# Kernel optimization log

Measured on AMD Instinct MI355X. Metric: run time of the kernel, lower is better.

Reference implementation:

```python
import jax, jax.numpy as jnp
import numpy as np

N_NODES = 10000
N_EDGES = 160000
NUM_REL = 16
NUM_BLOCKS = 32
BLOCK_SIZE = 4  # input_dim 128 = 32 * 4
INPUT_DIM = NUM_BLOCKS * BLOCK_SIZE


def setup_inputs() -> dict:
    key = jax.random.key(0)
    ks = jax.random.split(key, 6)
    std = float(np.sqrt(2.0) / (2 * BLOCK_SIZE))  # matches reset_parameters
    return {
        "x": jax.random.normal(ks[0], (N_NODES, INPUT_DIM), dtype=jnp.float32),
        "node_keep_mask": jnp.ones((N_NODES,), dtype=bool),
        "source": jax.random.randint(ks[1], (N_EDGES,), 0, N_NODES),
        "target": jax.random.randint(ks[2], (N_EDGES,), 0, N_NODES),
        "edge_type": jax.random.randint(ks[3], (N_EDGES,), 0, NUM_REL),
        "edge_weights": jax.random.uniform(ks[4], (N_EDGES,), dtype=jnp.float32),
        "blocks": jax.random.normal(ks[5], (NUM_REL + 1, NUM_BLOCKS, BLOCK_SIZE, BLOCK_SIZE), dtype=jnp.float32) * std,
    }


def reference(x, node_keep_mask, source, target, edge_type, edge_weights, blocks):
    n = x.shape[0]
    _, nb, bs, _ = blocks.shape
    xb = x.reshape(n, nb, bs)  # (N, B, bs)
    # self-loop transform with last block set; dropped-out nodes stay zero
    self_msg = jnp.einsum('nbi,bij->nbj', xb, blocks[-1])
    out = jnp.where(node_keep_mask[:, None, None], self_msg, 0.0)
    # symmetrize edges: messages flow both directions with same relation/weight
    src2 = jnp.concatenate([source, target])
    tgt2 = jnp.concatenate([target, source])
    et2 = jnp.concatenate([edge_type, edge_type])
    ew2 = jnp.concatenate([edge_weights, edge_weights])
    # per-edge block-diagonal matmul: gather relation blocks then 4x4 block GEMMs
    w_e = blocks[et2]                              # (2E, B, bs, bs)
    m = jnp.einsum('ebi,ebij->ebj', xb[src2], w_e)  # (2E, B, bs)
    m = m * ew2[:, None, None]
    out = out + jax.ops.segment_sum(m, tgt2, num_segments=n)
    return out.reshape(n, nb * bs)
```

## Files before the change

### kernel.cpp

```cpp
#include <hip/hip_runtime.h>

#define INPUT_DIM 128
#define NB 32
#define BS 4
#define CAP 128
#define WSTRIDE 20
#define GBLOCKS 1280


__global__ void scatter_kernel(const int* __restrict__ src, const int* __restrict__ tgt,
                               const int* __restrict__ etype, const float* __restrict__ ew,
                               int* __restrict__ counts, int2* __restrict__ msg,
                               int n_edges) {
    int i = blockIdx.x * blockDim.x + threadIdx.x;
    if (i >= 2 * n_edges) return;
    int e = (i < n_edges) ? i : i - n_edges;
    int s, t;
    if (i < n_edges) { s = src[e]; t = tgt[e]; }
    else             { s = tgt[e]; t = src[e]; }
    int pk = s | (etype[e] << 16);
    float w = ew[e];
    int pos = atomicAdd(&counts[t], 1);
    msg[t * CAP + pos] = make_int2(pk, __float_as_int(w));
}

__global__ __launch_bounds__(256, 4)
void gather_kernel(const float* __restrict__ x,
                   const int* __restrict__ keep,
                   const float* __restrict__ blocks,
                   const int* __restrict__ counts,
                   const int2* __restrict__ msg,
                   float* __restrict__ out, int n_nodes) {
    __shared__ float Wlds[16 * NB * WSTRIDE];

    for (int i = threadIdx.x; i < 16 * NB * 4; i += 256) {
        int blk = i >> 2;
        int row = i & 3;
        *(float4*)&Wlds[blk * WSTRIDE + row * 4] = ((const float4*)blocks)[i];
    }
    __syncthreads();

    int lane = threadIdx.x & 63;
    int b = lane & 31;
    int slot = lane >> 5;
    int wave_id = (blockIdx.x * blockDim.x + threadIdx.x) >> 6;
    int n_waves = gridDim.x * (blockDim.x >> 6);

    #define DO_MSG(PK, W)                                                     \
        {                                                                     \
            int s_ = (PK) & 0xFFFF;                                           \
            int r_ = (PK) >> 16;                                              \
            const float* Wp_ = &Wlds[(r_ * NB + b) * WSTRIDE];                \
            const float4 c0 = *(const float4*)(Wp_ + 0);                      \
            const float4 c1 = *(const float4*)(Wp_ + 4);                      \
            const float4 c2 = *(const float4*)(Wp_ + 8);                      \
            const float4 c3 = *(const float4*)(Wp_ + 12);                     \
            const float4 xv = *(const float4*)(x + (size_t)s_ * INPUT_DIM + b * BS); \
            acc.x += (W) * (xv.x * c0.x + xv.y * c1.x + xv.z * c2.x + xv.w * c3.x); \
            acc.y += (W) * (xv.x * c0.y + xv.y * c1.y + xv.z * c2.y + xv.w * c3.y); \
            acc.z += (W) * (xv.x * c0.z + xv.y * c1.z + xv.z * c2.z + xv.w * c3.z); \
            acc.w += (W) * (xv.x * c0.w + xv.y * c1.w + xv.z * c2.w + xv.w * c3.w); \
        }

    for (int n = wave_id; n < n_nodes; n += n_waves) {
        float4 acc = make_float4(0.f, 0.f, 0.f, 0.f);

        if (slot == 0 && keep[n] != 0) {
            const float4 xv = *(const float4*)(x + (size_t)n * INPUT_DIM + b * BS);
            const float* Wp = blocks + (((size_t)16 * NB + b) << 4);
            const float4 c0 = *(const float4*)(Wp + 0);
            const float4 c1 = *(const float4*)(Wp + 4);
            const float4 c2 = *(const float4*)(Wp + 8);
            const float4 c3 = *(const float4*)(Wp + 12);
            acc.x = xv.x * c0.x + xv.y * c1.x + xv.z * c2.x + xv.w * c3.x;
            acc.y = xv.x * c0.y + xv.y * c1.y + xv.z * c2.y + xv.w * c3.y;
            acc.z = xv.x * c0.z + xv.y * c1.z + xv.z * c2.z + xv.w * c3.z;
            acc.w = xv.x * c0.w + xv.y * c1.w + xv.z * c2.w + xv.w * c3.w;
        }

        int cnt = counts[n];
        int base = n * CAP;
        int p = 0;
        for (; p + 4 <= cnt; p += 4) {
            int2 m0 = msg[base + p + slot];
            int2 m1 = msg[base + p + 2 + slot];
            float w0 = __int_as_float(m0.y);
            float w1 = __int_as_float(m1.y);
            DO_MSG(m0.x, w0);
            DO_MSG(m1.x, w1);
        }
        for (; p < cnt; p += 2) {
            if (p + slot < cnt) {
                int2 m = msg[base + p + slot];
                DO_MSG(m.x, __int_as_float(m.y));
            }
        }

        acc.x += __shfl_xor(acc.x, 32, 64);
        acc.y += __shfl_xor(acc.y, 32, 64);
        acc.z += __shfl_xor(acc.z, 32, 64);
        acc.w += __shfl_xor(acc.w, 32, 64);

        if (slot == 0)
            *(float4*)(out + (size_t)n * INPUT_DIM + b * BS) = acc;
    }
    #undef DO_MSG
}

extern "C" void kernel_launch(void* const* d_in, const int* in_sizes, int n_in,
                              void* d_out, int out_size, void* d_ws, size_t ws_size,
                              hipStream_t stream) {
    const float* x       = (const float*)d_in[0];
    const int* km        = (const int*)d_in[1];
    const int* source    = (const int*)d_in[2];
    const int* target    = (const int*)d_in[3];
    const int* edge_type = (const int*)d_in[4];
    const float* edge_w  = (const float*)d_in[5];
    const float* blocks  = (const float*)d_in[6];
    float* out           = (float*)d_out;

    int n_nodes = in_sizes[0] / INPUT_DIM;
    int n_edges = in_sizes[2];
    int n_msg   = 2 * n_edges;

    int* counts = (int*)d_ws;
    int2* msg   = (int2*)((char*)d_ws + 65536);

    hipMemsetAsync(counts, 0, n_nodes * sizeof(int), stream);
    scatter_kernel<<<(n_msg + 255) / 256, 256, 0, stream>>>(
        source, target, edge_type, edge_w, counts, msg, n_edges);
    gather_kernel<<<GBLOCKS, 256, 0, stream>>>(
        x, km, blocks, counts, msg, out, n_nodes);
}
```

Baseline: 119.0 us.

## Convert x and relation blocks to fp16 and use packed dot2 in gather

A prep kernel converts x to packed fp16 and also performs the edge scatter, with each thread handling both directions of one edge. The gather kernel stores the relation blocks in LDS as transposed fp16 pairs and computes each 4x4 block product with fdot2 instructions, halving the bytes of the random x gathers. This lowers precision of the inputs and weights, which may exceed tolerance, and adds a conversion pass over x.

```diff
diff --git a/kernel.cpp b/kernel.cpp
--- a/kernel.cpp
+++ b/kernel.cpp
@@ -4,39 +4,77 @@
 #define NB 32
 #define BS 4
 #define CAP 128
-#define WSTRIDE 20
+#define WSTRIDE_U 12
 #define GBLOCKS 1280
 
+typedef _Float16 h2 __attribute__((ext_vector_type(2)));
+union HU { unsigned int u; h2 h; };
 
-__global__ void scatter_kernel(const int* __restrict__ src, const int* __restrict__ tgt,
-                               const int* __restrict__ etype, const float* __restrict__ ew,
-                               int* __restrict__ counts, int2* __restrict__ msg,
-                               int n_edges) {
+__device__ inline unsigned int pack_f16(float a, float b) {
+    HU v; v.h = h2{(_Float16)a, (_Float16)b}; return v.u;
+}
+__device__ inline h2 as_h2(unsigned int u) { HU v; v.u = u; return v.h; }
+
+#if defined(__has_builtin) && __has_builtin(__builtin_amdgcn_fdot2)
+__device__ inline float dot2(h2 a, h2 b, float c) {
+    return __builtin_amdgcn_fdot2(a, b, c, false);
+}
+#else
+__device__ inline float dot2(h2 a, h2 b, float c) {
+    return (float)a.x * (float)b.x + (float)a.y * (float)b.y + c;
+}
+#endif
+
+
+__global__ void prep_kernel(const float* __restrict__ x, unsigned int* __restrict__ xh,
+                            const int* __restrict__ src, const int* __restrict__ tgt,
+                            const int* __restrict__ etype, const float* __restrict__ ew,
+                            int* __restrict__ counts, int2* __restrict__ msg,
+                            int n_edges, int nx8) {
     int i = blockIdx.x * blockDim.x + threadIdx.x;
-    if (i >= 2 * n_edges) return;
-    int e = (i < n_edges) ? i : i - n_edges;
-    int s, t;
-    if (i < n_edges) { s = src[e]; t = tgt[e]; }
-    else             { s = tgt[e]; t = src[e]; }
-    int pk = s | (etype[e] << 16);
-    float w = ew[e];
-    int pos = atomicAdd(&counts[t], 1);
-    msg[t * CAP + pos] = make_int2(pk, __float_as_int(w));
+    if (i < nx8) {
+        const float4 a = *(const float4*)(x + (size_t)i * 8);
+        const float4 b = *(const float4*)(x + (size_t)i * 8 + 4);
+        uint4 o;
+        o.x = pack_f16(a.x, a.y);
+        o.y = pack_f16(a.z, a.w);
+        o.z = pack_f16(b.x, b.y);
+        o.w = pack_f16(b.z, b.w);
+        *(uint4*)(xh + (size_t)i * 4) = o;
+    }
+    if (i < n_edges) {
+        int s = src[i], t = tgt[i];
+        int pk_base = etype[i] << 16;
+        int wbits = __float_as_int(ew[i]);
+        int pf = atomicAdd(&counts[t], 1);
+        msg[t * CAP + pf] = make_int2(s | pk_base, wbits);
+        int pb = atomicAdd(&counts[s], 1);
+        msg[s * CAP + pb] = make_int2(t | pk_base, wbits);
+    }
 }
 
 __global__ __launch_bounds__(256, 4)
 void gather_kernel(const float* __restrict__ x,
+                   const unsigned int* __restrict__ xh,
                    const int* __restrict__ keep,
                    const float* __restrict__ blocks,
                    const int* __restrict__ counts,
                    const int2* __restrict__ msg,
                    float* __restrict__ out, int n_nodes) {
-    __shared__ float Wlds[16 * NB * WSTRIDE];
+    __shared__ unsigned int Wlds[16 * NB * WSTRIDE_U];
 
-    for (int i = threadIdx.x; i < 16 * NB * 4; i += 256) {
-        int blk = i >> 2;
-        int row = i & 3;
-        *(float4*)&Wlds[blk * WSTRIDE + row * 4] = ((const float4*)blocks)[i];
+    for (int bi = threadIdx.x; bi < 16 * NB; bi += 256) {
+        const float4 r0 = ((const float4*)blocks)[bi * 4 + 0];
+        const float4 r1 = ((const float4*)blocks)[bi * 4 + 1];
+        const float4 r2 = ((const float4*)blocks)[bi * 4 + 2];
+        const float4 r3 = ((const float4*)blocks)[bi * 4 + 3];
+        uint4 q0, q1;
+        q0.x = pack_f16(r0.x, r1.x); q0.y = pack_f16(r2.x, r3.x);
+        q0.z = pack_f16(r0.y, r1.y); q0.w = pack_f16(r2.y, r3.y);
+        q1.x = pack_f16(r0.z, r1.z); q1.y = pack_f16(r2.z, r3.z);
+        q1.z = pack_f16(r0.w, r1.w); q1.w = pack_f16(r2.w, r3.w);
+        *(uint4*)&Wlds[bi * WSTRIDE_U + 0] = q0;
+        *(uint4*)&Wlds[bi * WSTRIDE_U + 4] = q1;
     }
     __syncthreads();
 
@@ -50,16 +88,19 @@
         {                                                                     \
             int s_ = (PK) & 0xFFFF;                                           \
             int r_ = (PK) >> 16;                                              \
-            const float* Wp_ = &Wlds[(r_ * NB + b) * WSTRIDE];                \
-            const float4 c0 = *(const float4*)(Wp_ + 0);                      \
-            const float4 c1 = *(const float4*)(Wp_ + 4);                      \
-            const float4 c2 = *(const float4*)(Wp_ + 8);                      \
-            const float4 c3 = *(const float4*)(Wp_ + 12);                     \
-            const float4 xv = *(const float4*)(x + (size_t)s_ * INPUT_DIM + b * BS); \
-            acc.x += (W) * (xv.x * c0.x + xv.y * c1.x + xv.z * c2.x + xv.w * c3.x); \
-            acc.y += (W) * (xv.x * c0.y + xv.y * c1.y + xv.z * c2.y + xv.w * c3.y); \
-            acc.z += (W) * (xv.x * c0.z + xv.y * c1.z + xv.z * c2.z + xv.w * c3.z); \
-            acc.w += (W) * (xv.x * c0.w + xv.y * c1.w + xv.z * c2.w + xv.w * c3.w); \
+            const unsigned int* Wp_ = &Wlds[(r_ * NB + b) * WSTRIDE_U];       \
+            const uint4 q0 = *(const uint4*)(Wp_ + 0);                        \
+            const uint4 q1 = *(const uint4*)(Wp_ + 4);                        \
+            const uint2 xp = *(const uint2*)(xh + s_ * 64 + 2 * b);           \
+            const h2 xl = as_h2(xp.x), xh2 = as_h2(xp.y);                     \
+            float m0 = dot2(xl, as_h2(q0.x), dot2(xh2, as_h2(q0.y), 0.f));    \
+            float m1 = dot2(xl, as_h2(q0.z), dot2(xh2, as_h2(q0.w), 0.f));    \
+            float m2 = dot2(xl, as_h2(q1.x), dot2(xh2, as_h2(q1.y), 0.f));    \
+            float m3 = dot2(xl, as_h2(q1.z), dot2(xh2, as_h2(q1.w), 0.f));    \
+            acc.x += (W) * m0;                                                \
+            acc.y += (W) * m1;                                                \
+            acc.z += (W) * m2;                                                \
+            acc.w += (W) * m3;                                                \
         }
 
     for (int n = wave_id; n < n_nodes; n += n_waves) {
@@ -121,14 +162,16 @@
 
     int n_nodes = in_sizes[0] / INPUT_DIM;
     int n_edges = in_sizes[2];
-    int n_msg   = 2 * n_edges;
+    int nx8     = n_nodes * INPUT_DIM / 8;
 
-    int* counts = (int*)d_ws;
-    int2* msg   = (int2*)((char*)d_ws + 65536);
+    int* counts      = (int*)d_ws;
+    unsigned int* xh = (unsigned int*)((char*)d_ws + 65536);
+    int2* msg        = (int2*)((char*)d_ws + 65536 + (size_t)n_nodes * INPUT_DIM * 2);
 
     hipMemsetAsync(counts, 0, n_nodes * sizeof(int), stream);
-    scatter_kernel<<<(n_msg + 255) / 256, 256, 0, stream>>>(
-        source, target, edge_type, edge_w, counts, msg, n_edges);
+    int prep_threads = (n_edges > nx8) ? n_edges : nx8;
+    prep_kernel<<<(prep_threads + 255) / 256, 256, 0, stream>>>(
+        x, xh, source, target, edge_type, edge_w, counts, msg, n_edges, nx8);
     gather_kernel<<<GBLOCKS, 256, 0, stream>>>(
-        x, km, blocks, counts, msg, out, n_nodes);
+        x, xh, km, blocks, counts, msg, out, n_nodes);
 }
```

After: 112.1 us. 1.06x faster.
